# Kernel tuning notes

Measured on AMD Instinct MI355X. Metric: run time of the kernel, lower is better.

Reference implementation:

```python
import jax, jax.numpy as jnp
import numpy as np

N, E, DX, DT, H, C = 100000, 1000000, 126, 2, 8, 16
F_IN = DX + DT          # 128
F_OUT = H * C           # 128
NEG_SLOPE = 0.2


def setup_inputs() -> dict:
    key = jax.random.key(0)
    ks = jax.random.split(key, 12)
    s = 1.0 / np.sqrt(F_IN)
    return {
        "x": jax.random.normal(ks[0], (N, DX), jnp.float32),
        "time_feat": jax.random.normal(ks[1], (N, DT), jnp.float32),
        "edge_index": jax.random.randint(ks[2], (2, E), 0, N, jnp.int64),
        "Wl": jax.random.normal(ks[3], (F_IN, F_OUT), jnp.float32) * s,
        "Wr": jax.random.normal(ks[4], (F_IN, F_OUT), jnp.float32) * s,
        "att": jax.random.normal(ks[5], (H, C), jnp.float32) * 0.25,
        "bias_gat": jax.random.normal(ks[6], (F_OUT,), jnp.float32) * 0.01,
        "Ws": jax.random.normal(ks[7], (F_IN, F_OUT), jnp.float32) * s,
        "bs": jax.random.normal(ks[8], (F_OUT,), jnp.float32) * 0.01,
        "Wo": jax.random.normal(ks[9], (F_OUT, 1), jnp.float32) * (1.0 / np.sqrt(F_OUT)),
        "bo": jax.random.normal(ks[10], (1,), jnp.float32) * 0.01,
    }


def reference(x, time_feat, edge_index, Wl, Wr, att, bias_gat, Ws, bs, Wo, bo):
    raw = jnp.concatenate([x, time_feat], axis=1)            # [N, F_IN]
    n = raw.shape[0]
    # PyG GATv2Conv adds self-loops by default
    loops = jnp.arange(n, dtype=edge_index.dtype)
    src = jnp.concatenate([edge_index[0], loops])             # [E+N]
    dst = jnp.concatenate([edge_index[1], loops])

    xl = (raw @ Wl).reshape(n, H, C)                          # source transform
    xr = (raw @ Wr).reshape(n, H, C)                          # target transform

    m = xl[src] + xr[dst]                                     # [E+N, H, C]
    e = jnp.einsum('ehc,hc->eh', jax.nn.leaky_relu(m, NEG_SLOPE), att)

    # segment softmax over incoming edges of each destination node
    emax = jax.ops.segment_max(e, dst, num_segments=n)        # [N, H]
    ee = jnp.exp(e - emax[dst])
    denom = jax.ops.segment_sum(ee, dst, num_segments=n)
    alpha = ee / (denom[dst] + 1e-16)                         # [E+N, H]

    agg = jax.ops.segment_sum(alpha[:, :, None] * xl[src], dst, num_segments=n)
    graph_x = agg.reshape(n, F_OUT) + bias_gat                # concat heads

    skip_x = raw @ Ws + bs
    combined = jax.nn.elu(graph_x + skip_x)
    return jax.nn.sigmoid(combined @ Wo + bo)                 # [N, 1]
```

## Files before the change

kernel.cpp:

```cpp
#include <hip/hip_runtime.h>
#include <hip/hip_bf16.h>

#define NEG_SLOPE 0.2f
#define LOG2E 1.4426950408889634f
#define MAXDEG 64

#define NBUCK   512
#define BSHIFT  8
#define BUCKCAP 3072
#define CURSTRIDE 32

typedef __bf16 v8bf __attribute__((ext_vector_type(8)));
typedef float  v4f  __attribute__((ext_vector_type(4)));
typedef float  v2f  __attribute__((ext_vector_type(2)));

static __device__ __forceinline__ unsigned short f2b(float f) {
    unsigned u = __builtin_bit_cast(unsigned, f);
    u += 0x7FFFu + ((u >> 16) & 1u);
    return (unsigned short)(u >> 16);
}
static __device__ __forceinline__ void b2f2(unsigned u, float& lo, float& hi) {
    lo = __builtin_bit_cast(float, u << 16);
    hi = __builtin_bit_cast(float, u & 0xFFFF0000u);
}
static __device__ __forceinline__ void unpack8(uint4 u, float* f) {
    b2f2(u.x, f[0], f[1]); b2f2(u.y, f[2], f[3]);
    b2f2(u.z, f[4], f[5]); b2f2(u.w, f[6], f[7]);
}
static __device__ __forceinline__ v2f b2v2(unsigned u) {
    v2f r;
    r.x = __builtin_bit_cast(float, u << 16);
    r.y = __builtin_bit_cast(float, u & 0xFFFF0000u);
    return r;
}
static __device__ __forceinline__ void unpack8_v2(uint4 u, v2f* p) {
    p[0] = b2v2(u.x); p[1] = b2v2(u.y); p[2] = b2v2(u.z); p[3] = b2v2(u.w);
}

__global__ __launch_bounds__(256) void kA_prep(
    const float* __restrict__ Wl, const float* __restrict__ Wr,
    const float* __restrict__ Ws, unsigned short* __restrict__ Wt,
    int* __restrict__ cursors)
{
    int t = blockIdx.x * 256 + threadIdx.x;
    if (t < NBUCK) cursors[t * CURSTRIDE] = t * BUCKCAP;
    int nn = t >> 7, k = t & 127;
    const float* W = (nn < 128) ? Wl : ((nn < 256) ? Wr : Ws);
    Wt[t] = f2b(W[k * 128 + (nn & 127)]);
}

__global__ __launch_bounds__(256) void kB_part_gemm(
    const int* __restrict__ ei, int E,
    int* __restrict__ cursors, uint2* __restrict__ buck,
    const float* __restrict__ x, const float* __restrict__ tf,
    const unsigned short* __restrict__ Wt,
    const float* __restrict__ bg, const float* __restrict__ bs,
    unsigned short* __restrict__ xl_b, unsigned short* __restrict__ xr_b,
    unsigned short* __restrict__ sk_b, int N)
{
    __shared__ unsigned short lds[12672];
    const int tid = threadIdx.x;
    const int P1B = (E + 4095) >> 12;

    if ((int)blockIdx.x < P1B) {
        int* hist  = (int*)lds;
        int* bbase = hist + NBUCK;
        int* rctr  = hist + 2 * NBUCK;
        for (int b = tid; b < NBUCK; b += 256) { hist[b] = 0; rctr[b] = 0; }
        __syncthreads();

        #pragma unroll
        for (int h = 0; h < 2; ++h) {
            const int e0 = (int)blockIdx.x * 4096 + h * 2048 + tid;
            int d[8]; bool v[8];
            #pragma unroll
            for (int k = 0; k < 8; ++k) {
                int e = e0 + k * 256;
                v[k] = e < E;
                d[k] = ei[E + (v[k] ? e : 0)];
            }
            #pragma unroll
            for (int k = 0; k < 8; ++k)
                if (v[k]) atomicAdd(&hist[d[k] >> BSHIFT], 1);
        }
        __syncthreads();

        for (int b = tid; b < NBUCK; b += 256)
            if (hist[b] > 0)
                bbase[b] = __hip_atomic_fetch_add(&cursors[b * CURSTRIDE],
                                                  hist[b], __ATOMIC_RELAXED,
                                                  __HIP_MEMORY_SCOPE_AGENT);
        __syncthreads();

        #pragma unroll
        for (int h = 0; h < 2; ++h) {
            const int e0 = (int)blockIdx.x * 4096 + h * 2048 + tid;
            int s[8], d[8]; bool v[8];
            #pragma unroll
            for (int k = 0; k < 8; ++k) {
                int e = e0 + k * 256;
                v[k] = e < E;
                int ee = v[k] ? e : 0;
                s[k] = ei[ee];
                d[k] = ei[E + ee];
            }
            #pragma unroll
            for (int k = 0; k < 8; ++k) {
                if (v[k]) {
                    int b = d[k] >> BSHIFT;
                    int r = atomicAdd(&rctr[b], 1);
                    int idx = bbase[b] + r;
                    if (idx < (b + 1) * BUCKCAP)
                        buck[idx] = make_uint2((unsigned)s[k], (unsigned)d[k]);
                }
            }
        }
        return;
    }

    const int base = ((int)blockIdx.x - P1B) * 32;

    if (base + 32 <= N) {
        const float4* xp = reinterpret_cast<const float4*>(x + (size_t)base * 126);
        #pragma unroll
        for (int k = 0; k < 4; ++k) {
            int i = tid + k * 256;
            if (i < 1008) {
                int p = i / 63;
                int c = i - p * 63;
                float4 v = xp[i];
                int lf = c * 4;
                int f1 = lf + 2;
                int r0 = 2 * p + (lf >= 126 ? 1 : 0), c0 = lf - (lf >= 126 ? 126 : 0);
                int r1 = 2 * p + (f1 >= 126 ? 1 : 0), c1 = f1 - (f1 >= 126 ? 126 : 0);
                unsigned lo = (unsigned)f2b(v.x) | ((unsigned)f2b(v.y) << 16);
                unsigned hi = (unsigned)f2b(v.z) | ((unsigned)f2b(v.w) << 16);
                *reinterpret_cast<unsigned*>(&lds[r0 * 136 + c0]) = lo;
                *reinterpret_cast<unsigned*>(&lds[r1 * 136 + c1]) = hi;
            }
        }
    } else {
        #pragma unroll
        for (int t = 0; t < 8; ++t) {
            int idx = tid + t * 256;
            if (idx < 2016) {
                int row = idx / 63;
                int c = idx - row * 63;
                int gr = base + row; if (gr >= N) gr = N - 1;
                float2 v = *reinterpret_cast<const float2*>(x + (size_t)gr * 126 + 2 * c);
                unsigned u = (unsigned)f2b(v.x) | ((unsigned)f2b(v.y) << 16);
                *reinterpret_cast<unsigned*>(&lds[row * 136 + 2 * c]) = u;
            }
        }
    }
    if (tid < 32) {
        int gr = base + tid; if (gr >= N) gr = N - 1;
        float2 v = *reinterpret_cast<const float2*>(tf + (size_t)gr * 2);
        unsigned u = (unsigned)f2b(v.x) | ((unsigned)f2b(v.y) << 16);
        *reinterpret_cast<unsigned*>(&lds[tid * 136 + 126]) = u;
    }
    __syncthreads();

    const int wv = tid >> 6;
    const int lane = tid & 63;
    const int nidx = lane & 15, quad = lane >> 4;
    const int fbase = wv * 96;

    v4f acc[6][2];
    #pragma unroll
    for (int a = 0; a < 6; ++a)
        #pragma unroll
        for (int b = 0; b < 2; ++b) acc[a][b] = 0.0f;

    #pragma unroll
    for (int ks = 0; ks < 4; ++ks) {
        v8bf bfr[2];
        #pragma unroll
        for (int nf = 0; nf < 2; ++nf)
            bfr[nf] = *reinterpret_cast<const v8bf*>(
                &lds[(nf * 16 + nidx) * 136 + ks * 32 + quad * 8]);
        #pragma unroll
        for (int ft = 0; ft < 6; ++ft) {
            v8bf afr = *reinterpret_cast<const v8bf*>(
                Wt + (size_t)(fbase + ft * 16 + nidx) * 128 + ks * 32 + quad * 8);
            #pragma unroll
            for (int nf = 0; nf < 2; ++nf)
                acc[ft][nf] = __builtin_amdgcn_mfma_f32_16x16x32_bf16(
                    afr, bfr[nf], acc[ft][nf], 0, 0, 0);
        }
    }

    __syncthreads();

    #pragma unroll
    for (int ft = 0; ft < 6; ++ft) {
        const int f = fbase + ft * 16;
        const int arr = f >> 7;
        const int colb = (f & 127) + quad * 4;
        float b0 = 0.0f, b1 = 0.0f, b2 = 0.0f, b3 = 0.0f;
        if (arr == 2) {
            float4 v1 = *reinterpret_cast<const float4*>(bs + (f & 127) + quad * 4);
            float4 v2 = *reinterpret_cast<const float4*>(bg + (f & 127) + quad * 4);
            b0 = v1.x + v2.x; b1 = v1.y + v2.y; b2 = v1.z + v2.z; b3 = v1.w + v2.w;
        }
        #pragma unroll
        for (int nf = 0; nf < 2; ++nf) {
            const int nloc = nf * 16 + nidx;
            v4f v = acc[ft][nf];
            uint2 p;
            p.x = (unsigned)f2b(v[0] + b0) | ((unsigned)f2b(v[1] + b1) << 16);
            p.y = (unsigned)f2b(v[2] + b2) | ((unsigned)f2b(v[3] + b3) << 16);
            *reinterpret_cast<uint2*>(&lds[arr * 4224 + nloc * 132 + colb]) = p;
        }
    }
    __syncthreads();

    #pragma unroll
    for (int it = 0; it < 6; ++it) {
        int i = tid + it * 256;
        int arr = i >> 9;
        int idx = i & 511;
        int nloc = idx >> 4;
        int colh = (idx & 15) * 8;
        int node = base + nloc;
        if (node < N) {
            uint4 v = *reinterpret_cast<const uint4*>(&lds[arr * 4224 + nloc * 132 + colh]);
            unsigned short* dp = (arr == 0) ? xl_b : ((arr == 1) ? xr_b : sk_b);
            *reinterpret_cast<uint4*>(dp + (size_t)node * 128 + colh) = v;
        }
    }
}

__global__ __launch_bounds__(512) void kP2_slots(
    const uint2* __restrict__ buck, const int* __restrict__ cursors,
    int* __restrict__ counts, int* __restrict__ dense, int N)
{
    __shared__ int c[1 << BSHIFT];
    const int bb = (int)blockIdx.x;
    const int tid = threadIdx.x;
    if (tid < (1 << BSHIFT)) c[tid] = 0;
    __syncthreads();

    int cnt = cursors[bb * CURSTRIDE] - bb * BUCKCAP;
    if (cnt > BUCKCAP) cnt = BUCKCAP;
    const uint2* bp = buck + (size_t)bb * BUCKCAP;
    const int nb = bb << BSHIFT;

    const bool v0 = tid          < cnt, v1 = tid + 512  < cnt,
               v2 = tid + 1024  < cnt, v3 = tid + 1536  < cnt,
               v4 = tid + 2048  < cnt, v5 = tid + 2560  < cnt;
    uint2 z = make_uint2(0u, (unsigned)nb);
    uint2 p0 = v0 ? bp[tid]        : z, p1 = v1 ? bp[tid + 512]  : z,
          p2 = v2 ? bp[tid + 1024] : z, p3 = v3 ? bp[tid + 1536] : z,
          p4 = v4 ? bp[tid + 2048] : z, p5 = v5 ? bp[tid + 2560] : z;

    int s0 = v0 ? atomicAdd(&c[(int)p0.y - nb], 1) : MAXDEG;
    int s1 = v1 ? atomicAdd(&c[(int)p1.y - nb], 1) : MAXDEG;
    int s2 = v2 ? atomicAdd(&c[(int)p2.y - nb], 1) : MAXDEG;
    int s3 = v3 ? atomicAdd(&c[(int)p3.y - nb], 1) : MAXDEG;
    int s4 = v4 ? atomicAdd(&c[(int)p4.y - nb], 1) : MAXDEG;
    int s5 = v5 ? atomicAdd(&c[(int)p5.y - nb], 1) : MAXDEG;

    if (s0 < MAXDEG) dense[((size_t)p0.y << 6) + s0] = (int)p0.x;
    if (s1 < MAXDEG) dense[((size_t)p1.y << 6) + s1] = (int)p1.x;
    if (s2 < MAXDEG) dense[((size_t)p2.y << 6) + s2] = (int)p2.x;
    if (s3 < MAXDEG) dense[((size_t)p3.y << 6) + s3] = (int)p3.x;
    if (s4 < MAXDEG) dense[((size_t)p4.y << 6) + s4] = (int)p4.x;
    if (s5 < MAXDEG) dense[((size_t)p5.y << 6) + s5] = (int)p5.x;
    __syncthreads();

    if (tid < (1 << BSHIFT)) {
        int node = nb + tid;
        if (node < N) counts[node] = c[tid];
    }
}

__global__ __launch_bounds__(256, 6) void k2_aggfin(
    const int* __restrict__ counts, const int* __restrict__ dense,
    const unsigned short* __restrict__ xl_b,
    const unsigned short* __restrict__ xr_b,
    const unsigned short* __restrict__ sk_b,
    const float* __restrict__ att,
    const float* __restrict__ Wo, const float* __restrict__ bo,
    float* __restrict__ out, int N)
{
    const int node = __builtin_amdgcn_readfirstlane(
        (int)((blockIdx.x * (size_t)blockDim.x + threadIdx.x) >> 6));
    const int lane = threadIdx.x & 63;
    if (node >= N) return;
    const int j = lane & 15;
    const int g = lane >> 4;
    const int cb = j * 8;

    int cnt_raw = counts[node];
    int rawsrc = dense[((size_t)node << 6) + (lane == 0 ? 0 : lane - 1)];
    uint4 xru = *reinterpret_cast<const uint4*>(xr_b + (size_t)node * 128 + cb);
    uint4 sku = *reinterpret_cast<const uint4*>(sk_b + (size_t)node * 128 + cb);
    float4 a0 = *reinterpret_cast<const float4*>(att + cb);
    float4 a1 = *reinterpret_cast<const float4*>(att + cb + 4);

    v2f av2[4];
    av2[0] = (v2f){a0.x * LOG2E, a0.y * LOG2E};
    av2[1] = (v2f){a0.z * LOG2E, a0.w * LOG2E};
    av2[2] = (v2f){a1.x * LOG2E, a1.y * LOG2E};
    av2[3] = (v2f){a1.z * LOG2E, a1.w * LOG2E};
    v2f xr2[4];
    unpack8_v2(xru, xr2);

    int cnt = cnt_raw > 63 ? 63 : cnt_raw;
    const int total = cnt + 1;
    int src_all = (lane >= 1 && lane <= cnt) ? rawsrc : node;

    auto slotsrc = [&](int ii) -> int {
        int s = __shfl(src_all, ii & 63, 64);
        return (ii < total) ? s : node;
    };
    auto gather = [&](int src) -> uint4 {
        return *reinterpret_cast<const uint4*>(
            (const char*)xl_b + ((size_t)(unsigned)src << 8) + (cb << 1));
    };

    v2f acc2[4];
    #pragma unroll
    for (int c = 0; c < 4; ++c) acc2[c] = (v2f){0.0f, 0.0f};
    float den = 0.0f;

    auto proc = [&](uint4 cur, int it) {
        bool valid = (it * 4 + g) < total;
        v2f xl2[4];
        unpack8_v2(cur, xl2);
        v2f t2 = (v2f){0.0f, 0.0f};
        #pragma unroll
        for (int c = 0; c < 4; ++c) {
            v2f m = xl2[c] + xr2[c];
            v2f l = __builtin_elementwise_max(m, m * NEG_SLOPE);
            t2 = l * av2[c] + t2;
        }
        float t = t2.x + t2.y;
        t += __shfl_xor(t, 1, 64);
        float e = valid ? __builtin_amdgcn_exp2f(t) : 0.0f;
        v2f e2 = (v2f){e, e};
        #pragma unroll
        for (int c = 0; c < 4; ++c)
            acc2[c] = e2 * xl2[c] + acc2[c];
        den += e;
    };

    int   s0 = slotsrc(g),      s1 = slotsrc(4 + g),
          s2 = slotsrc(8 + g),  s3 = slotsrc(12 + g);
    uint4 u0 = gather(s0), u1 = gather(s1), u2 = gather(s2), u3 = gather(s3);

    const int iters = (total + 3) >> 2;
    for (int it = 0; it < iters; it += 4) {
        proc(u0, it);
        s0 = slotsrc((it + 4) * 4 + g); u0 = gather(s0);
        if (it + 1 < iters) {
            proc(u1, it + 1);
            s1 = slotsrc((it + 5) * 4 + g); u1 = gather(s1);
        }
        if (it + 2 < iters) {
            proc(u2, it + 2);
            s2 = slotsrc((it + 6) * 4 + g); u2 = gather(s2);
        }
        if (it + 3 < iters) {
            proc(u3, it + 3);
            s3 = slotsrc((it + 7) * 4 + g); u3 = gather(s3);
        }
    }

    #pragma unroll
    for (int c = 0; c < 4; ++c) {
        acc2[c].x += __shfl_xor(acc2[c].x, 16, 64);
        acc2[c].y += __shfl_xor(acc2[c].y, 16, 64);
        acc2[c].x += __shfl_xor(acc2[c].x, 32, 64);
        acc2[c].y += __shfl_xor(acc2[c].y, 32, 64);
    }
    den += __shfl_xor(den, 16, 64);
    den += __shfl_xor(den, 32, 64);

    float rd = 1.0f / (den + 1e-16f);
    v2f rd2 = (v2f){rd, rd};
    v2f sk2[4];
    unpack8_v2(sku, sk2);
    float4 w0 = *reinterpret_cast<const float4*>(Wo + cb);
    float4 w1 = *reinterpret_cast<const float4*>(Wo + cb + 4);
    float wvv[8] = {w0.x, w0.y, w0.z, w0.w, w1.x, w1.y, w1.z, w1.w};
    float s = 0.0f;
    #pragma unroll
    for (int c = 0; c < 4; ++c) {
        v2f gg2 = acc2[c] * rd2 + sk2[c];
        float g0 = gg2.x, g1 = gg2.y;
        float el0 = g0 > 0.0f ? g0 : (__builtin_amdgcn_exp2f(g0 * LOG2E) - 1.0f);
        float el1 = g1 > 0.0f ? g1 : (__builtin_amdgcn_exp2f(g1 * LOG2E) - 1.0f);
        s = fmaf(el0, wvv[2 * c], s);
        s = fmaf(el1, wvv[2 * c + 1], s);
    }
    s += __shfl_xor(s, 1, 64);
    s += __shfl_xor(s, 2, 64);
    s += __shfl_xor(s, 4, 64);
    s += __shfl_xor(s, 8, 64);
    if (lane == 0) {
        float z = s + bo[0];
        out[node] = 1.0f / (1.0f + __builtin_amdgcn_exp2f(-z * LOG2E));
    }
}

extern "C" void kernel_launch(void* const* d_in, const int* in_sizes, int n_in,
                              void* d_out, int out_size, void* d_ws, size_t ws_size,
                              hipStream_t stream) {
    const float* x   = (const float*)d_in[0];
    const float* tf  = (const float*)d_in[1];
    const int*   ei  = (const int*)  d_in[2];
    const float* Wl  = (const float*)d_in[3];
    const float* Wr  = (const float*)d_in[4];
    const float* att = (const float*)d_in[5];
    const float* bg  = (const float*)d_in[6];
    const float* Ws  = (const float*)d_in[7];
    const float* bs  = (const float*)d_in[8];
    const float* Wo  = (const float*)d_in[9];
    const float* bo  = (const float*)d_in[10];
    float* out = (float*)d_out;

    const int N = in_sizes[0] / 126;
    const int E = in_sizes[2] / 2;

    char* ws = (char*)d_ws;
    unsigned short* Wt   = (unsigned short*)ws; ws += (size_t)384 * 128 * 2;
    unsigned short* xl_b = (unsigned short*)ws; ws += (size_t)N * 128 * 2;
    unsigned short* xr_b = (unsigned short*)ws; ws += (size_t)N * 128 * 2;
    unsigned short* sk_b = (unsigned short*)ws; ws += (size_t)N * 128 * 2;
    int* counts = (int*)ws; ws += (size_t)N * 4;
    int* dense  = (int*)ws; ws += (size_t)N * MAXDEG * 4;
    int* cursors = (int*)ws; ws += (size_t)NBUCK * CURSTRIDE * 4;
    uint2* buck  = (uint2*)ws; ws += (size_t)NBUCK * BUCKCAP * 8;

    hipLaunchKernelGGL(kA_prep, dim3(192), dim3(256), 0, stream, Wl, Wr, Ws, Wt, cursors);
    const int P1B = (E + 4095) / 4096;
    const int GB = (N + 31) / 32;
    hipLaunchKernelGGL(kB_part_gemm, dim3(P1B + GB), dim3(256), 0, stream,
                       ei, E, cursors, buck, x, tf, Wt, bg, bs,
                       xl_b, xr_b, sk_b, N);
    const int P2B = (N + (1 << BSHIFT) - 1) >> BSHIFT;
    hipLaunchKernelGGL(kP2_slots, dim3(P2B), dim3(512), 0, stream,
                       buck, cursors, counts, dense, N);
    hipLaunchKernelGGL(k2_aggfin, dim3((N + 3) / 4), dim3(256), 0, stream,
                       counts, dense, xl_b, xr_b, sk_b, att, Wo, bo, out, N);
}
```

Before: 234.7 us.

## Fuse slot bucketing with attention aggregation using LDS adjacency

Merges the slot-assignment kernel and the per-node aggregation kernel into one. Each block builds its bucket's per-node source lists in shared memory and then has its 8 waves loop over the 256 nodes to do the softmax-weighted gather and output. This removes the global dense/count arrays, their write and read traffic, and one launch. In exchange the grid shrinks to a few hundred large blocks with heavy LDS use, which lowers occupancy and latency hiding for the random gathers.

```diff
diff --git a/kernel.cpp b/kernel.cpp
--- a/kernel.cpp
+++ b/kernel.cpp
@@ -22,10 +22,6 @@
 static __device__ __forceinline__ void b2f2(unsigned u, float& lo, float& hi) {
     lo = __builtin_bit_cast(float, u << 16);
     hi = __builtin_bit_cast(float, u & 0xFFFF0000u);
-}
-static __device__ __forceinline__ void unpack8(uint4 u, float* f) {
-    b2f2(u.x, f[0], f[1]); b2f2(u.y, f[2], f[3]);
-    b2f2(u.z, f[4], f[5]); b2f2(u.w, f[6], f[7]);
 }
 static __device__ __forceinline__ v2f b2v2(unsigned u) {
     v2f r;
@@ -231,52 +227,8 @@
     }
 }
 
-__global__ __launch_bounds__(512) void kP2_slots(
+__global__ __launch_bounds__(512) void kP2k2(
     const uint2* __restrict__ buck, const int* __restrict__ cursors,
-    int* __restrict__ counts, int* __restrict__ dense, int N)
-{
-    __shared__ int c[1 << BSHIFT];
-    const int bb = (int)blockIdx.x;
-    const int tid = threadIdx.x;
-    if (tid < (1 << BSHIFT)) c[tid] = 0;
-    __syncthreads();
-
-    int cnt = cursors[bb * CURSTRIDE] - bb * BUCKCAP;
-    if (cnt > BUCKCAP) cnt = BUCKCAP;
-    const uint2* bp = buck + (size_t)bb * BUCKCAP;
-    const int nb = bb << BSHIFT;
-
-    const bool v0 = tid          < cnt, v1 = tid + 512  < cnt,
-               v2 = tid + 1024  < cnt, v3 = tid + 1536  < cnt,
-               v4 = tid + 2048  < cnt, v5 = tid + 2560  < cnt;
-    uint2 z = make_uint2(0u, (unsigned)nb);
-    uint2 p0 = v0 ? bp[tid]        : z, p1 = v1 ? bp[tid + 512]  : z,
-          p2 = v2 ? bp[tid + 1024] : z, p3 = v3 ? bp[tid + 1536] : z,
-          p4 = v4 ? bp[tid + 2048] : z, p5 = v5 ? bp[tid + 2560] : z;
-
-    int s0 = v0 ? atomicAdd(&c[(int)p0.y - nb], 1) : MAXDEG;
-    int s1 = v1 ? atomicAdd(&c[(int)p1.y - nb], 1) : MAXDEG;
-    int s2 = v2 ? atomicAdd(&c[(int)p2.y - nb], 1) : MAXDEG;
-    int s3 = v3 ? atomicAdd(&c[(int)p3.y - nb], 1) : MAXDEG;
-    int s4 = v4 ? atomicAdd(&c[(int)p4.y - nb], 1) : MAXDEG;
-    int s5 = v5 ? atomicAdd(&c[(int)p5.y - nb], 1) : MAXDEG;
-
-    if (s0 < MAXDEG) dense[((size_t)p0.y << 6) + s0] = (int)p0.x;
-    if (s1 < MAXDEG) dense[((size_t)p1.y << 6) + s1] = (int)p1.x;
-    if (s2 < MAXDEG) dense[((size_t)p2.y << 6) + s2] = (int)p2.x;
-    if (s3 < MAXDEG) dense[((size_t)p3.y << 6) + s3] = (int)p3.x;
-    if (s4 < MAXDEG) dense[((size_t)p4.y << 6) + s4] = (int)p4.x;
-    if (s5 < MAXDEG) dense[((size_t)p5.y << 6) + s5] = (int)p5.x;
-    __syncthreads();
-
-    if (tid < (1 << BSHIFT)) {
-        int node = nb + tid;
-        if (node < N) counts[node] = c[tid];
-    }
-}
-
-__global__ __launch_bounds__(256, 6) void k2_aggfin(
-    const int* __restrict__ counts, const int* __restrict__ dense,
     const unsigned short* __restrict__ xl_b,
     const unsigned short* __restrict__ xr_b,
     const unsigned short* __restrict__ sk_b,
@@ -284,124 +236,166 @@
     const float* __restrict__ Wo, const float* __restrict__ bo,
     float* __restrict__ out, int N)
 {
-    const int node = __builtin_amdgcn_readfirstlane(
-        (int)((blockIdx.x * (size_t)blockDim.x + threadIdx.x) >> 6));
-    const int lane = threadIdx.x & 63;
-    if (node >= N) return;
+    __shared__ int c[1 << BSHIFT];
+    __shared__ int slots[(1 << BSHIFT) * MAXDEG];
+    const int bb = (int)blockIdx.x;
+    const int tid = threadIdx.x;
+    if (tid < (1 << BSHIFT)) c[tid] = 0;
+    __syncthreads();
+
+    int cnt = cursors[bb * CURSTRIDE] - bb * BUCKCAP;
+    if (cnt > BUCKCAP) cnt = BUCKCAP;
+    const uint2* bp = buck + (size_t)bb * BUCKCAP;
+    const int nb = bb << BSHIFT;
+
+    {
+        const bool v0 = tid          < cnt, v1 = tid + 512  < cnt,
+                   v2 = tid + 1024  < cnt, v3 = tid + 1536  < cnt,
+                   v4 = tid + 2048  < cnt, v5 = tid + 2560  < cnt;
+        uint2 z = make_uint2(0u, (unsigned)nb);
+        uint2 p0 = v0 ? bp[tid]        : z, p1 = v1 ? bp[tid + 512]  : z,
+              p2 = v2 ? bp[tid + 1024] : z, p3 = v3 ? bp[tid + 1536] : z,
+              p4 = v4 ? bp[tid + 2048] : z, p5 = v5 ? bp[tid + 2560] : z;
+
+        int s0 = v0 ? atomicAdd(&c[(int)p0.y - nb], 1) : MAXDEG;
+        int s1 = v1 ? atomicAdd(&c[(int)p1.y - nb], 1) : MAXDEG;
+        int s2 = v2 ? atomicAdd(&c[(int)p2.y - nb], 1) : MAXDEG;
+        int s3 = v3 ? atomicAdd(&c[(int)p3.y - nb], 1) : MAXDEG;
+        int s4 = v4 ? atomicAdd(&c[(int)p4.y - nb], 1) : MAXDEG;
+        int s5 = v5 ? atomicAdd(&c[(int)p5.y - nb], 1) : MAXDEG;
+
+        if (s0 < MAXDEG) slots[((int)p0.y - nb) * MAXDEG + s0] = (int)p0.x;
+        if (s1 < MAXDEG) slots[((int)p1.y - nb) * MAXDEG + s1] = (int)p1.x;
+        if (s2 < MAXDEG) slots[((int)p2.y - nb) * MAXDEG + s2] = (int)p2.x;
+        if (s3 < MAXDEG) slots[((int)p3.y - nb) * MAXDEG + s3] = (int)p3.x;
+        if (s4 < MAXDEG) slots[((int)p4.y - nb) * MAXDEG + s4] = (int)p4.x;
+        if (s5 < MAXDEG) slots[((int)p5.y - nb) * MAXDEG + s5] = (int)p5.x;
+    }
+    __syncthreads();
+
+    const int wv = tid >> 6;
+    const int lane = tid & 63;
     const int j = lane & 15;
     const int g = lane >> 4;
     const int cb = j * 8;
 
-    int cnt_raw = counts[node];
-    int rawsrc = dense[((size_t)node << 6) + (lane == 0 ? 0 : lane - 1)];
-    uint4 xru = *reinterpret_cast<const uint4*>(xr_b + (size_t)node * 128 + cb);
-    uint4 sku = *reinterpret_cast<const uint4*>(sk_b + (size_t)node * 128 + cb);
     float4 a0 = *reinterpret_cast<const float4*>(att + cb);
     float4 a1 = *reinterpret_cast<const float4*>(att + cb + 4);
-
+    float4 w0 = *reinterpret_cast<const float4*>(Wo + cb);
+    float4 w1 = *reinterpret_cast<const float4*>(Wo + cb + 4);
     v2f av2[4];
     av2[0] = (v2f){a0.x * LOG2E, a0.y * LOG2E};
     av2[1] = (v2f){a0.z * LOG2E, a0.w * LOG2E};
     av2[2] = (v2f){a1.x * LOG2E, a1.y * LOG2E};
     av2[3] = (v2f){a1.z * LOG2E, a1.w * LOG2E};
-    v2f xr2[4];
-    unpack8_v2(xru, xr2);
-
-    int cnt = cnt_raw > 63 ? 63 : cnt_raw;
-    const int total = cnt + 1;
-    int src_all = (lane >= 1 && lane <= cnt) ? rawsrc : node;
-
-    auto slotsrc = [&](int ii) -> int {
-        int s = __shfl(src_all, ii & 63, 64);
-        return (ii < total) ? s : node;
-    };
+    float wvv[8] = {w0.x, w0.y, w0.z, w0.w, w1.x, w1.y, w1.z, w1.w};
+    const float bo0 = bo[0];
+
     auto gather = [&](int src) -> uint4 {
         return *reinterpret_cast<const uint4*>(
             (const char*)xl_b + ((size_t)(unsigned)src << 8) + (cb << 1));
     };
 
-    v2f acc2[4];
-    #pragma unroll
-    for (int c = 0; c < 4; ++c) acc2[c] = (v2f){0.0f, 0.0f};
-    float den = 0.0f;
-
-    auto proc = [&](uint4 cur, int it) {
-        bool valid = (it * 4 + g) < total;
-        v2f xl2[4];
-        unpack8_v2(cur, xl2);
-        v2f t2 = (v2f){0.0f, 0.0f};
-        #pragma unroll
-        for (int c = 0; c < 4; ++c) {
-            v2f m = xl2[c] + xr2[c];
-            v2f l = __builtin_elementwise_max(m, m * NEG_SLOPE);
-            t2 = l * av2[c] + t2;
-        }
-        float t = t2.x + t2.y;
-        t += __shfl_xor(t, 1, 64);
-        float e = valid ? __builtin_amdgcn_exp2f(t) : 0.0f;
-        v2f e2 = (v2f){e, e};
-        #pragma unroll
-        for (int c = 0; c < 4; ++c)
-            acc2[c] = e2 * xl2[c] + acc2[c];
-        den += e;
-    };
-
-    int   s0 = slotsrc(g),      s1 = slotsrc(4 + g),
-          s2 = slotsrc(8 + g),  s3 = slotsrc(12 + g);
-    uint4 u0 = gather(s0), u1 = gather(s1), u2 = gather(s2), u3 = gather(s3);
-
-    const int iters = (total + 3) >> 2;
-    for (int it = 0; it < iters; it += 4) {
-        proc(u0, it);
-        s0 = slotsrc((it + 4) * 4 + g); u0 = gather(s0);
-        if (it + 1 < iters) {
-            proc(u1, it + 1);
-            s1 = slotsrc((it + 5) * 4 + g); u1 = gather(s1);
-        }
-        if (it + 2 < iters) {
-            proc(u2, it + 2);
-            s2 = slotsrc((it + 6) * 4 + g); u2 = gather(s2);
-        }
-        if (it + 3 < iters) {
-            proc(u3, it + 3);
-            s3 = slotsrc((it + 7) * 4 + g); u3 = gather(s3);
-        }
-    }
-
-    #pragma unroll
-    for (int c = 0; c < 4; ++c) {
-        acc2[c].x += __shfl_xor(acc2[c].x, 16, 64);
-        acc2[c].y += __shfl_xor(acc2[c].y, 16, 64);
-        acc2[c].x += __shfl_xor(acc2[c].x, 32, 64);
-        acc2[c].y += __shfl_xor(acc2[c].y, 32, 64);
-    }
-    den += __shfl_xor(den, 16, 64);
-    den += __shfl_xor(den, 32, 64);
-
-    float rd = 1.0f / (den + 1e-16f);
-    v2f rd2 = (v2f){rd, rd};
-    v2f sk2[4];
-    unpack8_v2(sku, sk2);
-    float4 w0 = *reinterpret_cast<const float4*>(Wo + cb);
-    float4 w1 = *reinterpret_cast<const float4*>(Wo + cb + 4);
-    float wvv[8] = {w0.x, w0.y, w0.z, w0.w, w1.x, w1.y, w1.z, w1.w};
-    float s = 0.0f;
-    #pragma unroll
-    for (int c = 0; c < 4; ++c) {
-        v2f gg2 = acc2[c] * rd2 + sk2[c];
-        float g0 = gg2.x, g1 = gg2.y;
-        float el0 = g0 > 0.0f ? g0 : (__builtin_amdgcn_exp2f(g0 * LOG2E) - 1.0f);
-        float el1 = g1 > 0.0f ? g1 : (__builtin_amdgcn_exp2f(g1 * LOG2E) - 1.0f);
-        s = fmaf(el0, wvv[2 * c], s);
-        s = fmaf(el1, wvv[2 * c + 1], s);
-    }
-    s += __shfl_xor(s, 1, 64);
-    s += __shfl_xor(s, 2, 64);
-    s += __shfl_xor(s, 4, 64);
-    s += __shfl_xor(s, 8, 64);
-    if (lane == 0) {
-        float z = s + bo[0];
-        out[node] = 1.0f / (1.0f + __builtin_amdgcn_exp2f(-z * LOG2E));
+    for (int rep = 0; rep < (1 << BSHIFT) / 8; ++rep) {
+        const int nloc = (rep << 3) + wv;
+        const int node = nb + nloc;
+        if (node >= N) break;
+
+        int ccnt = c[nloc]; if (ccnt > 63) ccnt = 63;
+        const int total = ccnt + 1;
+        const int* sl = slots + nloc * MAXDEG;
+
+        uint4 xru = *reinterpret_cast<const uint4*>(xr_b + (size_t)node * 128 + cb);
+        v2f xr2[4];
+        unpack8_v2(xru, xr2);
+
+        auto slotsrc = [&](int ii) -> int {
+            bool valid = (ii > 0) && (ii < total);
+            int s = sl[valid ? ii - 1 : 0];
+            return valid ? s : node;
+        };
+
+        v2f acc2[4];
+        #pragma unroll
+        for (int cc = 0; cc < 4; ++cc) acc2[cc] = (v2f){0.0f, 0.0f};
+        float den = 0.0f;
+
+        auto proc = [&](uint4 cur, int it) {
+            bool valid = (it * 4 + g) < total;
+            v2f xl2[4];
+            unpack8_v2(cur, xl2);
+            v2f t2 = (v2f){0.0f, 0.0f};
+            #pragma unroll
+            for (int cc = 0; cc < 4; ++cc) {
+                v2f m = xl2[cc] + xr2[cc];
+                v2f l = __builtin_elementwise_max(m, m * NEG_SLOPE);
+                t2 = l * av2[cc] + t2;
+            }
+            float t = t2.x + t2.y;
+            t += __shfl_xor(t, 1, 64);
+            float e = valid ? __builtin_amdgcn_exp2f(t) : 0.0f;
+            v2f e2 = (v2f){e, e};
+            #pragma unroll
+            for (int cc = 0; cc < 4; ++cc)
+                acc2[cc] = e2 * xl2[cc] + acc2[cc];
+            den += e;
+        };
+
+        int   s0 = slotsrc(g),      s1 = slotsrc(4 + g),
+              s2 = slotsrc(8 + g),  s3 = slotsrc(12 + g);
+        uint4 u0 = gather(s0), u1 = gather(s1), u2 = gather(s2), u3 = gather(s3);
+
+        const int iters = (total + 3) >> 2;
+        for (int it = 0; it < iters; it += 4) {
+            proc(u0, it);
+            s0 = slotsrc((it + 4) * 4 + g); u0 = gather(s0);
+            if (it + 1 < iters) {
+                proc(u1, it + 1);
+                s1 = slotsrc((it + 5) * 4 + g); u1 = gather(s1);
+            }
+            if (it + 2 < iters) {
+                proc(u2, it + 2);
+                s2 = slotsrc((it + 6) * 4 + g); u2 = gather(s2);
+            }
+            if (it + 3 < iters) {
+                proc(u3, it + 3);
+                s3 = slotsrc((it + 7) * 4 + g); u3 = gather(s3);
+            }
+        }
+
+        #pragma unroll
+        for (int cc = 0; cc < 4; ++cc) {
+            acc2[cc].x += __shfl_xor(acc2[cc].x, 16, 64);
+            acc2[cc].y += __shfl_xor(acc2[cc].y, 16, 64);
+            acc2[cc].x += __shfl_xor(acc2[cc].x, 32, 64);
+            acc2[cc].y += __shfl_xor(acc2[cc].y, 32, 64);
+        }
+        den += __shfl_xor(den, 16, 64);
+        den += __shfl_xor(den, 32, 64);
+
+        float rd = 1.0f / (den + 1e-16f);
+        v2f rd2 = (v2f){rd, rd};
+        uint4 sku = *reinterpret_cast<const uint4*>(sk_b + (size_t)node * 128 + cb);
+        v2f sk2[4];
+        unpack8_v2(sku, sk2);
+        float s = 0.0f;
+        #pragma unroll
+        for (int cc = 0; cc < 4; ++cc) {
+            v2f gg2 = acc2[cc] * rd2 + sk2[cc];
+            float g0 = gg2.x, g1 = gg2.y;
+            float el0 = g0 > 0.0f ? g0 : (__builtin_amdgcn_exp2f(g0 * LOG2E) - 1.0f);
+            float el1 = g1 > 0.0f ? g1 : (__builtin_amdgcn_exp2f(g1 * LOG2E) - 1.0f);
+            s = fmaf(el0, wvv[2 * cc], s);
+            s = fmaf(el1, wvv[2 * cc + 1], s);
+        }
+        s += __shfl_xor(s, 1, 64);
+        s += __shfl_xor(s, 2, 64);
+        s += __shfl_xor(s, 4, 64);
+        s += __shfl_xor(s, 8, 64);
+        if (lane == 0) {
+            float z = s + bo0;
+            out[node] = 1.0f / (1.0f + __builtin_amdgcn_exp2f(-z * LOG2E));
+        }
     }
 }
 
@@ -429,8 +423,6 @@
     unsigned short* xl_b = (unsigned short*)ws; ws += (size_t)N * 128 * 2;
     unsigned short* xr_b = (unsigned short*)ws; ws += (size_t)N * 128 * 2;
     unsigned short* sk_b = (unsigned short*)ws; ws += (size_t)N * 128 * 2;
-    int* counts = (int*)ws; ws += (size_t)N * 4;
-    int* dense  = (int*)ws; ws += (size_t)N * MAXDEG * 4;
     int* cursors = (int*)ws; ws += (size_t)NBUCK * CURSTRIDE * 4;
     uint2* buck  = (uint2*)ws; ws += (size_t)NBUCK * BUCKCAP * 8;
 
@@ -441,8 +433,6 @@
                        ei, E, cursors, buck, x, tf, Wt, bg, bs,
                        xl_b, xr_b, sk_b, N);
     const int P2B = (N + (1 << BSHIFT) - 1) >> BSHIFT;
-    hipLaunchKernelGGL(kP2_slots, dim3(P2B), dim3(512), 0, stream,
-                       buck, cursors, counts, dense, N);
-    hipLaunchKernelGGL(k2_aggfin, dim3((N + 3) / 4), dim3(256), 0, stream,
-                       counts, dense, xl_b, xr_b, sk_b, att, Wo, bo, out, N);
-}
+    hipLaunchKernelGGL(kP2k2, dim3(P2B), dim3(512), 0, stream,
+                       buck, cursors, xl_b, xr_b, sk_b, att, Wo, bo, out, N);
+}
```

Result: slower. 257.6 us (+9.8%).
